# Kernel tuning notes

Measured on AMD Instinct MI355X. Metric: run time of the kernel, lower is better.

The kernel has to match this reference:

```python
import jax, jax.numpy as jnp
import numpy as np

N_NODES = 40000
N_EDGES = 480000
MULT = 64
NUM_SPECIES = 5
N_BASIS = 8
MLP_HIDDEN = 64
AVG_NEIGH = 12.0

INV8 = float(1.0 / np.sqrt(8.0))
INV64 = float(1.0 / np.sqrt(64.0))
INV128 = float(1.0 / np.sqrt(128.0))


def _poly_envelope(x):
    # e3nn.poly_envelope(5, 2) == DimeNet-style cutoff with p=6:
    # f(0)=1, first 5 derivatives zero at 0, f and 2 derivatives zero at 1.
    u = 1.0 - 28.0 * x**6 + 48.0 * x**7 - 21.0 * x**8
    return jnp.where(x < 1.0, u, 0.0)


def setup_inputs() -> dict:
    key = jax.random.key(0)
    ks = jax.random.split(key, 15)
    vectors = jax.random.uniform(ks[0], (N_EDGES, 3), jnp.float32, -0.5, 0.5)
    node_scalars = jax.random.normal(ks[1], (N_NODES, MULT), jnp.float32)
    node_vectors = jax.random.normal(ks[2], (N_NODES, MULT, 3), jnp.float32)
    node_specie = jax.random.randint(ks[3], (N_NODES,), 0, NUM_SPECIES)
    senders = jax.random.randint(ks[4], (N_EDGES,), 0, N_NODES)
    receivers = jax.random.randint(ks[5], (N_EDGES,), 0, N_NODES)
    # learned params (e3nn Linear weights ~ N(0,1), fwd divides by sqrt(fan_in))
    W_up_s = jax.random.normal(ks[6], (MULT, MULT), jnp.float32)
    W_up_v = jax.random.normal(ks[7], (MULT, MULT), jnp.float32)
    W_skip_s = jax.random.normal(ks[8], (NUM_SPECIES, MULT, 2 * MULT), jnp.float32)
    W_skip_v = jax.random.normal(ks[9], (NUM_SPECIES, MULT, MULT), jnp.float32)
    W_mlp1 = jax.random.normal(ks[10], (N_BASIS, MLP_HIDDEN), jnp.float32)
    W_mlp2 = jax.random.normal(ks[11], (MLP_HIDDEN, MLP_HIDDEN), jnp.float32)
    W_mlp3 = jax.random.normal(ks[12], (MLP_HIDDEN, 4 * MULT), jnp.float32)
    W_down_s = jax.random.normal(ks[13], (2 * MULT, 2 * MULT), jnp.float32)
    W_down_v = jax.random.normal(ks[14], (2 * MULT, MULT), jnp.float32)
    return dict(vectors=vectors, node_scalars=node_scalars, node_vectors=node_vectors,
                node_specie=node_specie, senders=senders, receivers=receivers,
                W_up_s=W_up_s, W_up_v=W_up_v, W_skip_s=W_skip_s, W_skip_v=W_skip_v,
                W_mlp1=W_mlp1, W_mlp2=W_mlp2, W_mlp3=W_mlp3,
                W_down_s=W_down_s, W_down_v=W_down_v)


def reference(vectors, node_scalars, node_vectors, node_specie, senders, receivers,
              W_up_s, W_up_v, W_skip_s, W_skip_v, W_mlp1, W_mlp2, W_mlp3,
              W_down_s, W_down_v):
    N = node_scalars.shape[0]
    # self-connection: species-indexed linear ('skip_tp'), output 128x0e + 64x1o
    sc_s = jnp.einsum('ni,nio->no', node_scalars, W_skip_s[node_specie]) * INV64
    sc_v = jnp.einsum('nic,nio->noc', node_vectors, W_skip_v[node_specie]) * INV64
    # linear_up (irreps-wise linear, 64x0e+64x1o -> same)
    h_s = (node_scalars @ W_up_s) * INV64
    h_v = jnp.einsum('nic,io->noc', node_vectors, W_up_v) * INV64
    # gather by sender
    m_s = h_s[senders]                       # [E,64]
    m_v = h_v[senders]                       # [E,64,3]
    # spherical harmonics l=1, normalize=True, component norm: sqrt(3)*r_hat
    lengths = jnp.linalg.norm(vectors, axis=1, keepdims=True)   # [E,1]
    safe_len = jnp.where(lengths == 0.0, 1.0, lengths)
    Y = jnp.sqrt(3.0) * vectors / safe_len                      # [E,3]
    # sparse CG tensor product (component norm): 0e x 1o -> 1o, 1o x 1o -> 0e
    tp_1o = m_s[:, :, None] * Y[:, None, :]                     # [E,64,3]
    tp_0e = jnp.einsum('eic,ec->ei', m_v, Y) / jnp.sqrt(3.0)    # [E,64]
    # concatenate + regroup -> 128x0e + 128x1o
    msg_s = jnp.concatenate([m_s, tp_0e], axis=1)               # [E,128]
    msg_v = jnp.concatenate([m_v, tp_1o], axis=1)               # [E,128,3]
    # radial basis (bessel, x_max=1) * smooth envelope
    k = jnp.arange(1, N_BASIS + 1, dtype=jnp.float32)
    bes = jnp.sqrt(2.0) * jnp.sin(k * jnp.pi * safe_len) / safe_len  # [E,8]
    rb = jnp.where(lengths == 0.0, 0.0, bes * _poly_envelope(lengths))
    h = jax.nn.swish((rb @ W_mlp1) * INV8)
    h = jax.nn.swish((h @ W_mlp2) * INV64)
    mix = (h @ W_mlp3) * INV64                                  # [E,256]
    msg_s = msg_s * mix[:, :128]
    msg_v = msg_v * mix[:, 128:, None]
    # scatter-add to receivers, normalize by sqrt(avg_num_neighbors)
    inv_sqrt_nn = 1.0 / np.sqrt(AVG_NEIGH)
    agg_s = jax.ops.segment_sum(msg_s, receivers, num_segments=N) * inv_sqrt_nn
    agg_v = jax.ops.segment_sum(msg_v, receivers, num_segments=N) * inv_sqrt_nn
    # linear_down to 128x0e + 64x1o, plus self-connection
    d_s = (agg_s @ W_down_s) * INV128 + sc_s                    # [N,128]
    d_v = jnp.einsum('nic,io->noc', agg_v, W_down_v) * INV128 + sc_v  # [N,64,3]
    # gate: first 64 scalars kept (swish), last 64 gate the vectors (swish)
    out_s = jax.nn.swish(d_s[:, :MULT])
    gates = jax.nn.swish(d_s[:, MULT:])
    out_v = d_v * gates[:, :, None]
    return jnp.concatenate([out_s, out_v.reshape(N, MULT * 3)], axis=1)  # [N,256]
```

## Files before the change

### kernel.cpp

```cpp
#include <hip/hip_runtime.h>
#include <hip/hip_bf16.h>

#define N_NODES 40000
#define N_EDGES 480000
#define SEG 2
#define SEG_E (N_EDGES / SEG)
#define SEG_TILES (SEG_E / 16)
#define SCAN_BLOCKS 157
#define TPW 4

typedef short bf16x8 __attribute__((ext_vector_type(8)));
typedef float f32x4 __attribute__((ext_vector_type(4)));

__device__ __forceinline__ float bf2f(__hip_bfloat16 x) { return __bfloat162float(x); }

__device__ __forceinline__ float swishf(float x) { return x / (1.0f + __expf(-x)); }

__device__ __forceinline__ float bflo(unsigned u) { union { unsigned u; float f; } w; w.u = u << 16; return w.f; }
__device__ __forceinline__ float bfhi(unsigned u) { union { unsigned u; float f; } w; w.u = u & 0xffff0000u; return w.f; }
__device__ __forceinline__ float bfu(unsigned short u) { union { unsigned u; float f; } w; w.u = ((unsigned)u) << 16; return w.f; }

__device__ __forceinline__ unsigned short f2bf_bits(float x) {
    union { __hip_bfloat16 h; unsigned short u; } c; c.h = __float2bfloat16(x); return c.u;
}

__constant__ const float INV8 = 0.35355339059327373f;
__constant__ const float INV64 = 0.125f;
__constant__ const float INV128 = 0.08838834764831845f;
__constant__ const float INV_NN = 0.2886751345948129f;
__constant__ const float SQRT2 = 1.4142135623730951f;
__constant__ const float SQRT3 = 1.7320508075688772f;
__constant__ const float INV_SQRT3 = 0.5773502691896258f;
__constant__ const float PI_F = 3.14159265358979323846f;

__device__ __forceinline__ float LDf(const void* p, size_t i, bool f32) {
    float v;
    if (f32) v = ((const float*)p)[i];
    else     v = bf2f(((const __hip_bfloat16*)p)[i]);
    return v;
}
__device__ __forceinline__ void load_f8r(const void* p, size_t i, bool f32, float* out) {
    if (f32) {
        const float4* q4 = (const float4*)((const float*)p + i);
        float4 a = q4[0], b = q4[1];
        out[0] = a.x; out[1] = a.y; out[2] = a.z; out[3] = a.w;
        out[4] = b.x; out[5] = b.y; out[6] = b.z; out[7] = b.w;
    } else {
        bf16x8 v = *(const bf16x8*)((const unsigned short*)p + i);
        #pragma unroll
        for (int j = 0; j < 8; j++) out[j] = bfu((unsigned short)v[j]);
    }
}

__global__ void detect_kernel(const unsigned short* __restrict__ w, int* __restrict__ flag) {
    int lane = threadIdx.x;
    int cnt = 0;
    for (int i = lane; i < 2048; i += 64) {
        unsigned e = (w[2 * i] >> 7) & 0xFF;
        if (e >= 110 && e <= 133) cnt++;
    }
    #pragma unroll
    for (int off = 32; off > 0; off >>= 1) cnt += __shfl_down(cnt, off, 64);
    if (lane == 0) *flag = (cnt > 1024) ? 1 : 0;
}

__global__ __launch_bounds__(256) void wprep_kernel(
    const void* __restrict__ W_up_s, const void* __restrict__ W_up_v,
    const void* __restrict__ W_skip_s, const void* __restrict__ W_skip_v,
    const void* __restrict__ W_down_s, const void* __restrict__ W_down_v,
    const void* __restrict__ W_mlp2, const void* __restrict__ W_mlp3,
    unsigned short* __restrict__ Wup_sq, unsigned short* __restrict__ Wup_vq,
    unsigned short* __restrict__ Wq_s, unsigned short* __restrict__ Wq_v,
    unsigned short* __restrict__ W2q, unsigned short* __restrict__ W3q,
    const int* __restrict__ flag)
{
    bool f32 = (*flag == 0);
    const float SC = INV128 * INV_NN;
    int gid = blockIdx.x * 256 + threadIdx.x;
    int gs = gridDim.x * 256;
    for (int i = gid; i < 4096; i += gs) {
        int o = i & 63, k = i >> 6;
        Wup_sq[o * 72 + k] = f2bf_bits(LDf(W_up_s, k * 64 + o, f32) * INV64);
        Wup_vq[o * 72 + k] = f2bf_bits(LDf(W_up_v, k * 64 + o, f32) * INV64);
    }
    for (int i = gid; i < 5 * 128 * 192; i += gs) {
        int sp = i / 24576, r = i - sp * 24576;
        int o = r / 192, k = r - o * 192;
        float w = (k < 128) ? LDf(W_down_s, k * 128 + o, f32) * SC
                            : LDf(W_skip_s, sp * 8192 + (k - 128) * 128 + o, f32) * INV64;
        Wq_s[sp * 25600 + o * 200 + k] = f2bf_bits(w);
    }
    for (int i = gid; i < 5 * 64 * 192; i += gs) {
        int sp = i / 12288, r = i - sp * 12288;
        int o = r / 192, k = r - o * 192;
        float w = (k < 128) ? LDf(W_down_v, k * 64 + o, f32) * SC
                            : LDf(W_skip_v, sp * 4096 + (k - 128) * 64 + o, f32) * INV64;
        Wq_v[sp * 12800 + o * 200 + k] = f2bf_bits(w);
    }
    for (int i = gid; i < 16384; i += gs) {
        int o = i & 255, k = i >> 8;
        W3q[o * 72 + k] = f2bf_bits(LDf(W_mlp3, k * 256 + o, f32));
    }
    for (int i = gid; i < 4096; i += gs) {
        int o = i & 63, k = i >> 6;
        W2q[o * 72 + k] = f2bf_bits(LDf(W_mlp2, k * 64 + o, f32));
    }
}

__global__ __launch_bounds__(256) void hist_kernel(const int* __restrict__ receivers,
                                                   int* __restrict__ cnt) {
    int e = blockIdx.x * 256 + threadIdx.x;
    if (e < N_EDGES) atomicAdd(&cnt[receivers[e]], 1);
}

__global__ __launch_bounds__(256) void partial_kernel(const int* __restrict__ cnt,
                                                      int* __restrict__ partials) {
    __shared__ int red[4];
    int idx = blockIdx.x * 256 + threadIdx.x;
    int v = (idx < N_NODES) ? cnt[idx] : 0;
    #pragma unroll
    for (int off = 32; off > 0; off >>= 1) v += __shfl_down(v, off, 64);
    int wave = threadIdx.x >> 6, lane = threadIdx.x & 63;
    if (lane == 0) red[wave] = v;
    __syncthreads();
    if (threadIdx.x == 0) partials[blockIdx.x] = red[0] + red[1] + red[2] + red[3];
}

__global__ __launch_bounds__(256) void scanp_kernel(const int* __restrict__ partials,
                                                    int* __restrict__ pscan) {
    __shared__ int buf[256];
    int t = threadIdx.x;
    int v = (t < SCAN_BLOCKS) ? partials[t] : 0;
    buf[t] = v;
    __syncthreads();
    for (int off = 1; off < 256; off <<= 1) {
        int tmp = (t >= off) ? buf[t - off] : 0;
        __syncthreads();
        buf[t] += tmp;
        __syncthreads();
    }
    if (t < SCAN_BLOCKS) pscan[t] = buf[t] - v;
}

__global__ __launch_bounds__(256) void offs_kernel(const int* __restrict__ cnt,
                                                   const int* __restrict__ pscan,
                                                   int* __restrict__ offs,
                                                   int* __restrict__ cursor) {
    __shared__ int buf[256];
    int b = blockIdx.x, t = threadIdx.x;
    int idx = b * 256 + t;
    int v = (idx < N_NODES) ? cnt[idx] : 0;
    buf[t] = v;
    __syncthreads();
    for (int off = 1; off < 256; off <<= 1) {
        int tmp = (t >= off) ? buf[t - off] : 0;
        __syncthreads();
        buf[t] += tmp;
        __syncthreads();
    }
    int exc = buf[t] - v + pscan[b];
    if (idx < N_NODES) { offs[idx] = exc; cursor[idx] = exc; }
    if (idx == N_NODES - 1) offs[N_NODES] = exc + v;
}

__global__ __launch_bounds__(256) void scatter_kernel(const int* __restrict__ receivers,
                                                      const int* __restrict__ senders,
                                                      const void* __restrict__ vectors,
                                                      int* __restrict__ cursor,
                                                      int* __restrict__ sorted_snd,
                                                      unsigned short* __restrict__ yq,
                                                      unsigned short* __restrict__ rbq,
                                                      const int* __restrict__ flag) {
    bool f32 = (*flag == 0);
    int e = blockIdx.x * 256 + threadIdx.x;
    if (e < N_EDGES) {
        float vx = LDf(vectors, (size_t)e * 3 + 0, f32);
        float vy = LDf(vectors, (size_t)e * 3 + 1, f32);
        float vz = LDf(vectors, (size_t)e * 3 + 2, f32);
        float len2 = vx * vx + vy * vy + vz * vz;
        float len = sqrtf(len2);
        float Yx = 0.f, Yy = 0.f, Yz = 0.f;
        float rb[8];
        if (len > 0.f) {
            float inv = 1.f / len;
            Yx = SQRT3 * vx * inv; Yy = SQRT3 * vy * inv; Yz = SQRT3 * vz * inv;
            float x6 = len2 * len2 * len2;
            float env = (len < 1.f) ? fmaf(x6, fmaf(len, fmaf(len, -21.f, 48.f), -28.f), 1.f) : 0.f;
            float c = SQRT2 * inv * env;
            #pragma unroll
            for (int k = 0; k < 8; k++) rb[k] = c * __sinf((float)(k + 1) * PI_F * len);
        } else {
            #pragma unroll
            for (int k = 0; k < 8; k++) rb[k] = 0.f;
        }
        int p = atomicAdd(&cursor[receivers[e]], 1);
        sorted_snd[p] = senders[e];
        uint2 yw;
        yw.x = f2bf_bits(Yx) | ((unsigned)f2bf_bits(Yy) << 16);
        yw.y = f2bf_bits(Yz);
        *(uint2*)(yq + (size_t)p * 4) = yw;
        bf16x8 r8;
        #pragma unroll
        for (int k = 0; k < 8; k++) r8[k] = (short)f2bf_bits(rb[k]);
        *(bf16x8*)(rbq + (size_t)p * 8) = r8;
    }
}

__global__ __launch_bounds__(256) void hist5_kernel(const int* __restrict__ specie,
                                                    int* __restrict__ cnt5) {
    int n = blockIdx.x * 256 + threadIdx.x;
    int lane = threadIdx.x & 63;
    int sp = (n < N_NODES) ? specie[n] : -1;
    #pragma unroll
    for (int s = 0; s < 5; s++) {
        unsigned long long mask = __ballot(sp == s);
        if (mask != 0ull) {
            int leader = __builtin_ctzll(mask);
            if (lane == leader) atomicAdd(&cnt5[s], __popcll(mask));
        }
    }
}

__global__ void scan5_kernel(const int* __restrict__ cnt5, int* __restrict__ sp_offs,
                             int* __restrict__ cursor5, int* __restrict__ tile_info) {
    if (threadIdx.x != 0 || blockIdx.x != 0) return;
    int run = 0, tb = 0;
    for (int s = 0; s < 5; s++) {
        sp_offs[s] = run; cursor5[s] = run;
        tile_info[s] = tb;
        int c = cnt5[s];
        int T = (c + 15) >> 4;
        tile_info[8 + s] = T;
        tb += (T + 3) >> 2;
        run += c;
    }
    sp_offs[5] = run;
    tile_info[5] = tb;
}

__global__ __launch_bounds__(256) void scatter5_kernel(const int* __restrict__ specie,
                                                       int* __restrict__ cursor5,
                                                       int* __restrict__ sorted_node) {
    int n = blockIdx.x * 256 + threadIdx.x;
    int lane = threadIdx.x & 63;
    int sp = (n < N_NODES) ? specie[n] : -1;
    #pragma unroll
    for (int s = 0; s < 5; s++) {
        unsigned long long mask = __ballot(sp == s);
        if (mask != 0ull) {
            int leader = __builtin_ctzll(mask);
            int base = 0;
            if (lane == leader) base = atomicAdd(&cursor5[s], __popcll(mask));
            base = __shfl(base, leader);
            if (sp == s) {
                int prefix = __popcll(mask & ((1ull << lane) - 1ull));
                sorted_node[base + prefix] = n;
            }
        }
    }
}

__global__ __launch_bounds__(256) void node_up_kernel(
    const void* __restrict__ node_scalars,
    const void* __restrict__ node_vectors,
    const unsigned short* __restrict__ Wup_sq,
    const unsigned short* __restrict__ Wup_vq,
    unsigned short* __restrict__ hbuf,
    unsigned short* __restrict__ ns_b,
    unsigned short* __restrict__ nv_t,
    const int* __restrict__ flag)
{
    bool f32 = (*flag == 0);
    __shared__ __align__(16) unsigned short WsT[64 * 72];
    __shared__ __align__(16) unsigned short WvT[64 * 72];
    int tid = threadIdx.x;
    for (int i = tid; i < 576; i += 256) {
        ((uint4*)WsT)[i] = ((const uint4*)Wup_sq)[i];
        ((uint4*)WvT)[i] = ((const uint4*)Wup_vq)[i];
    }
    __syncthreads();
    int wave = tid >> 6, lane = tid & 63;
    int m = lane & 15, q = lane >> 4;
    int base = (blockIdx.x * 4 + wave) * 16;

    f32x4 accS[4];
    f32x4 accV[3][4];
    #pragma unroll
    for (int t = 0; t < 4; t++) {
        accS[t] = f32x4{0.f, 0.f, 0.f, 0.f};
        #pragma unroll
        for (int c = 0; c < 3; c++) accV[c][t] = f32x4{0.f, 0.f, 0.f, 0.f};
    }

    #pragma unroll
    for (int kk = 0; kk < 2; kk++) {
        int i0 = kk * 32 + 8 * q;
        float fs[8];
        load_f8r(node_scalars, (size_t)(base + m) * 64 + i0, f32, fs);
        bf16x8 aS;
        #pragma unroll
        for (int j = 0; j < 8; j++) aS[j] = (short)f2bf_bits(fs[j]);
        *(bf16x8*)(ns_b + (size_t)(base + m) * 64 + i0) = aS;
        float fv[24];
        size_t vbase = (size_t)(base + m) * 192 + (size_t)i0 * 3;
        load_f8r(node_vectors, vbase,      f32, fv);
        load_f8r(node_vectors, vbase + 8,  f32, fv + 8);
        load_f8r(node_vectors, vbase + 16, f32, fv + 16);
        bf16x8 aV[3];
        #pragma unroll
        for (int c = 0; c < 3; c++) {
            #pragma unroll
            for (int j = 0; j < 8; j++) aV[c][j] = (short)f2bf_bits(fv[3 * j + c]);
            *(bf16x8*)(nv_t + (size_t)c * N_NODES * 64 + (size_t)(base + m) * 64 + i0) = aV[c];
        }
        #pragma unroll
        for (int t = 0; t < 4; t++) {
            bf16x8 bS = *(const bf16x8*)(WsT + (16 * t + m) * 72 + kk * 32 + 8 * q);
            bf16x8 bV = *(const bf16x8*)(WvT + (16 * t + m) * 72 + kk * 32 + 8 * q);
            accS[t]    = __builtin_amdgcn_mfma_f32_16x16x32_bf16(aS,    bS, accS[t],    0, 0, 0);
            accV[0][t] = __builtin_amdgcn_mfma_f32_16x16x32_bf16(aV[0], bV, accV[0][t], 0, 0, 0);
            accV[1][t] = __builtin_amdgcn_mfma_f32_16x16x32_bf16(aV[1], bV, accV[1][t], 0, 0, 0);
            accV[2][t] = __builtin_amdgcn_mfma_f32_16x16x32_bf16(aV[2], bV, accV[2][t], 0, 0, 0);
        }
    }
    #pragma unroll
    for (int t = 0; t < 4; t++) {
        #pragma unroll
        for (int r = 0; r < 4; r++) {
            uint2 pk;
            pk.x = (unsigned)f2bf_bits(accS[t][r])    | ((unsigned)f2bf_bits(accV[0][t][r]) << 16);
            pk.y = (unsigned)f2bf_bits(accV[1][t][r]) | ((unsigned)f2bf_bits(accV[2][t][r]) << 16);
            *(uint2*)(hbuf + (size_t)(base + 4 * q + r) * 256 + (16 * t + m) * 4) = pk;
        }
    }
}

__global__ __launch_bounds__(512) void mlp_kernel(
    const unsigned short* __restrict__ rbq,
    const void* __restrict__ W1,
    const unsigned short* __restrict__ W2q,
    const unsigned short* __restrict__ W3q,
    unsigned short* __restrict__ mixp,
    int p_lo,
    const int* __restrict__ flag)
{
    bool f32 = (*flag == 0);
    __shared__ __align__(16) unsigned short W3T[256 * 72];
    __shared__ __align__(16) unsigned short W2T[64 * 72];
    __shared__ unsigned short hbl[8 * 64 * 18];
    int tid = threadIdx.x;
    for (int i = tid; i < 2304; i += 512) ((uint4*)W3T)[i] = ((const uint4*)W3q)[i];
    for (int i = tid; i < 576; i += 512)  ((uint4*)W2T)[i] = ((const uint4*)W2q)[i];
    __syncthreads();
    int wave = tid >> 6, lane = tid & 63;
    int m = lane & 15, q = lane >> 4;
    unsigned short* hb = hbl + wave * (64 * 18);
    f32x4 zero4 = {0.f, 0.f, 0.f, 0.f};

    bf16x8 a1f[4];
    #pragma unroll
    for (int t = 0; t < 4; t++) {
        #pragma unroll
        for (int j = 0; j < 8; j++) a1f[t][j] = 0;
        if (q == 0) {
            #pragma unroll
            for (int j = 0; j < 8; j++)
                a1f[t][j] = (short)f2bf_bits(LDf(W1, j * 64 + 16 * t + m, f32));
        }
    }

    int tile0 = (blockIdx.x * 8 + wave) * TPW;
    #pragma unroll 1
    for (int tt = 0; tt < TPW; tt++) {
        int tile = tile0 + tt;
        if (tile >= SEG_TILES) break;
        int p = p_lo + tile * 16 + m;

        bf16x8 b_rb;
        #pragma unroll
        for (int j = 0; j < 8; j++) b_rb[j] = 0;
        if (q == 0) b_rb = *(const bf16x8*)(rbq + (size_t)p * 8);

        #pragma unroll
        for (int t = 0; t < 4; t++) {
            f32x4 c = __builtin_amdgcn_mfma_f32_16x16x32_bf16(a1f[t], b_rb, zero4, 0, 0, 0);
            #pragma unroll
            for (int r = 0; r < 4; r++)
                hb[(16 * t + 4 * q + r) * 18 + m] = f2bf_bits(swishf(c[r] * INV8));
        }
        bf16x8 b2[2];
        #pragma unroll
        for (int h = 0; h < 2; h++)
            #pragma unroll
            for (int j = 0; j < 8; j++)
                b2[h][j] = (short)hb[(32 * h + 8 * q + j) * 18 + m];
        #pragma unroll
        for (int t = 0; t < 4; t++) {
            bf16x8 a0 = *(const bf16x8*)(W2T + (16 * t + m) * 72 + 8 * q);
            bf16x8 a1 = *(const bf16x8*)(W2T + (16 * t + m) * 72 + 32 + 8 * q);
            f32x4 c = __builtin_amdgcn_mfma_f32_16x16x32_bf16(a0, b2[0], zero4, 0, 0, 0);
            c = __builtin_amdgcn_mfma_f32_16x16x32_bf16(a1, b2[1], c, 0, 0, 0);
            #pragma unroll
            for (int r = 0; r < 4; r++)
                hb[(16 * t + 4 * q + r) * 18 + m] = f2bf_bits(swishf(c[r] * INV64));
        }
        bf16x8 b3[2];
        #pragma unroll
        for (int h = 0; h < 2; h++)
            #pragma unroll
            for (int j = 0; j < 8; j++)
                b3[h][j] = (short)hb[(32 * h + 8 * q + j) * 18 + m];
        size_t ebase = ((size_t)(tile * 16 + m)) * 256;
        #pragma unroll
        for (int t3p = 0; t3p < 4; t3p++) {
            f32x4 cg[4];
            #pragma unroll
            for (int g = 0; g < 4; g++) {
                int t3 = t3p + 4 * g;
                bf16x8 a0 = *(const bf16x8*)(W3T + (16 * t3 + m) * 72 + 8 * q);
                bf16x8 a1 = *(const bf16x8*)(W3T + (16 * t3 + m) * 72 + 32 + 8 * q);
                f32x4 c = __builtin_amdgcn_mfma_f32_16x16x32_bf16(a0, b3[0], zero4, 0, 0, 0);
                cg[g] = __builtin_amdgcn_mfma_f32_16x16x32_bf16(a1, b3[1], c, 0, 0, 0);
            }
            #pragma unroll
            for (int r = 0; r < 4; r += 2) {
                uint4 w;
                w.x = f2bf_bits(cg[0][r] * INV64)     | ((unsigned)f2bf_bits(cg[1][r] * INV64) << 16);
                w.y = f2bf_bits(cg[2][r] * INV64)     | ((unsigned)f2bf_bits(cg[3][r] * INV64) << 16);
                w.z = f2bf_bits(cg[0][r + 1] * INV64) | ((unsigned)f2bf_bits(cg[1][r + 1] * INV64) << 16);
                w.w = f2bf_bits(cg[2][r + 1] * INV64) | ((unsigned)f2bf_bits(cg[3][r + 1] * INV64) << 16);
                *(uint4*)(mixp + ebase + (size_t)(16 * t3p + 4 * q + r) * 4) = w;
            }
        }
    }
}

__global__ __launch_bounds__(256) void agg_kernel(
    const unsigned short* __restrict__ hbuf,
    const int* __restrict__ sorted_snd,
    const unsigned short* __restrict__ mixp,
    const unsigned short* __restrict__ yq,
    const int* __restrict__ offs,
    unsigned short* __restrict__ agg_s_b,
    unsigned short* __restrict__ agg_v_b,
    int slo, int shi)
{
    int tid = threadIdx.x, wave = tid >> 6, lane = tid & 63;
    int n = blockIdx.x * 4 + wave;
    if (n >= N_NODES) return;
    int beg = __builtin_amdgcn_readfirstlane(offs[n]);
    int end = __builtin_amdgcn_readfirstlane(offs[n + 1]);
    int lo = beg > slo ? beg : slo;
    int hi = end < shi ? end : shi;
    bool owner = (beg >= slo && beg < shi) || (beg >= shi && shi == N_EDGES);
    if (!owner && hi <= lo) return;
    unsigned short* aS = agg_s_b + (size_t)n * 128;
    unsigned short* aV = agg_v_b + (size_t)n * 384;
    float s0, s1, v0, v1, v2, v3, v4, v5;
    if (owner) {
        s0 = s1 = v0 = v1 = v2 = v3 = v4 = v5 = 0.f;
    } else {
        s0 = bfu(aS[lane]); s1 = bfu(aS[64 + lane]);
        v0 = bfu(aV[lane]); v1 = bfu(aV[64 + lane]); v2 = bfu(aV[128 + lane]);
        v3 = bfu(aV[192 + lane]); v4 = bfu(aV[256 + lane]); v5 = bfu(aV[320 + lane]);
    }
    for (int chunk = lo; chunk < hi; chunk += 64) {
        int cc = hi - chunk; if (cc > 64) cc = 64;
        int sv = (lane < cc) ? sorted_snd[chunk + lane] : 0;
        int i = 0;
        for (; i + 3 < cc; i += 4) {
            uint2 h[4], mxw[4], yw[4];
            #pragma unroll
            for (int u = 0; u < 4; u++) {
                int snd = __builtin_amdgcn_readlane(sv, i + u);
                int p = chunk + i + u;
                h[u]   = *(const uint2*)(hbuf + (size_t)snd * 256 + lane * 4);
                mxw[u] = *(const uint2*)(mixp + (size_t)(p - slo) * 256 + lane * 4);
                yw[u]  = *(const uint2*)(yq + (size_t)p * 4);
            }
            #pragma unroll
            for (int u = 0; u < 4; u++) {
                float m_s = bflo(h[u].x), mv0 = bfhi(h[u].x), mv1 = bflo(h[u].y), mv2 = bfhi(h[u].y);
                float mix0 = bflo(mxw[u].x), mix1 = bfhi(mxw[u].x);
                float mix2 = bflo(mxw[u].y), mix3 = bfhi(mxw[u].y);
                float Yx = bflo(yw[u].x), Yy = bfhi(yw[u].x), Yz = bflo(yw[u].y);
                float tp0 = (mv0 * Yx + mv1 * Yy + mv2 * Yz) * INV_SQRT3;
                s0 = fmaf(m_s, mix0, s0);
                s1 = fmaf(tp0, mix1, s1);
                float t1 = m_s * mix3;
                v0 = fmaf(mv0, mix2, v0); v1 = fmaf(t1, Yx, v1);
                v2 = fmaf(mv1, mix2, v2); v3 = fmaf(t1, Yy, v3);
                v4 = fmaf(mv2, mix2, v4); v5 = fmaf(t1, Yz, v5);
            }
        }
        for (; i < cc; i++) {
            int snd = __builtin_amdgcn_readlane(sv, i);
            int p = chunk + i;
            uint2 hbv = *(const uint2*)(hbuf + (size_t)snd * 256 + lane * 4);
            uint2 mxw = *(const uint2*)(mixp + (size_t)(p - slo) * 256 + lane * 4);
            uint2 yw  = *(const uint2*)(yq + (size_t)p * 4);
            float m_s = bflo(hbv.x), mv0 = bfhi(hbv.x), mv1 = bflo(hbv.y), mv2 = bfhi(hbv.y);
            float mix0 = bflo(mxw.x), mix1 = bfhi(mxw.x);
            float mix2 = bflo(mxw.y), mix3 = bfhi(mxw.y);
            float Yx = bflo(yw.x), Yy = bfhi(yw.x), Yz = bflo(yw.y);
            float tp0 = (mv0 * Yx + mv1 * Yy + mv2 * Yz) * INV_SQRT3;
            s0 = fmaf(m_s, mix0, s0);
            s1 = fmaf(tp0, mix1, s1);
            float t1 = m_s * mix3;
            v0 = fmaf(mv0, mix2, v0); v1 = fmaf(t1, Yx, v1);
            v2 = fmaf(mv1, mix2, v2); v3 = fmaf(t1, Yy, v3);
            v4 = fmaf(mv2, mix2, v4); v5 = fmaf(t1, Yz, v5);
        }
    }
    aS[lane] = f2bf_bits(s0); aS[64 + lane] = f2bf_bits(s1);
    aV[lane] = f2bf_bits(v0); aV[64 + lane] = f2bf_bits(v1); aV[128 + lane] = f2bf_bits(v2);
    aV[192 + lane] = f2bf_bits(v3); aV[256 + lane] = f2bf_bits(v4); aV[320 + lane] = f2bf_bits(v5);
}

__global__ __launch_bounds__(256) void node_final_kernel(
    const unsigned short* __restrict__ Wq_s,
    const unsigned short* __restrict__ Wq_v,
    const unsigned short* __restrict__ ns_b,
    const unsigned short* __restrict__ nv_t,
    const unsigned short* __restrict__ agg_s_b,
    const unsigned short* __restrict__ agg_v_b,
    const int* __restrict__ sorted_node,
    const int* __restrict__ sp_offs,
    const int* __restrict__ tile_info,
    void* __restrict__ out,
    const int* __restrict__ flag)
{
    bool f32 = (*flag == 0);
    int b = blockIdx.x;
    if (b >= tile_info[5]) return;
    __shared__ __align__(16) unsigned short As[128 * 200];
    __shared__ __align__(16) unsigned short Av[64 * 200];
    int sp = 0;
    #pragma unroll
    for (int s = 1; s < 5; s++) if (b >= tile_info[s]) sp = s;
    int tid = threadIdx.x;
    const uint4* ps = (const uint4*)(Wq_s + (size_t)sp * 25600);
    for (int i = tid; i < 3200; i += 256) ((uint4*)As)[i] = ps[i];
    const uint4* pv = (const uint4*)(Wq_v + (size_t)sp * 12800);
    for (int i = tid; i < 1600; i += 256) ((uint4*)Av)[i] = pv[i];
    __syncthreads();
    int wave = tid >> 6, lane = tid & 63;
    int m = lane & 15, q = lane >> 4;
    int T = tile_info[8 + sp];
    int tl = (b - tile_info[sp]) * 4 + wave;
    if (tl >= T) return;
    int row = sp_offs[sp] + tl * 16;
    int cnt = sp_offs[sp + 1] - row; if (cnt > 16) cnt = 16;
    int mm = (m < cnt) ? m : 0;
    int node = sorted_node[row + mm];

    bf16x8 bs[6];
    {
        const unsigned short* a = agg_s_b + (size_t)node * 128;
        #pragma unroll
        for (int f = 0; f < 4; f++) bs[f] = *(const bf16x8*)(a + f * 32 + q * 8);
        const unsigned short* s = ns_b + (size_t)node * 64;
        #pragma unroll
        for (int f = 0; f < 2; f++) bs[4 + f] = *(const bf16x8*)(s + f * 32 + q * 8);
    }
    bf16x8 bv[3][6];
    #pragma unroll
    for (int c = 0; c < 3; c++) {
        const unsigned short* a = agg_v_b + (size_t)node * 384 + c * 128;
        #pragma unroll
        for (int f = 0; f < 4; f++) bv[c][f] = *(const bf16x8*)(a + f * 32 + q * 8);
        const unsigned short* s = nv_t + (size_t)c * N_NODES * 64 + (size_t)node * 64;
        #pragma unroll
        for (int f = 0; f < 2; f++) bv[c][4 + f] = *(const bf16x8*)(s + f * 32 + q * 8);
    }
    f32x4 z4 = {0.f, 0.f, 0.f, 0.f};
    float gate[4][4];
    #pragma unroll
    for (int t = 0; t < 4; t++) {
        f32x4 c = z4;
        #pragma unroll
        for (int f = 0; f < 6; f++) {
            bf16x8 a = *(const bf16x8*)(As + (16 * (4 + t) + m) * 200 + f * 32 + q * 8);
            c = __builtin_amdgcn_mfma_f32_16x16x32_bf16(a, bs[f], c, 0, 0, 0);
        }
        #pragma unroll
        for (int r = 0; r < 4; r++) gate[t][r] = swishf(c[r]);
    }
    #pragma unroll
    for (int t = 0; t < 4; t++) {
        f32x4 c = z4;
        #pragma unroll
        for (int f = 0; f < 6; f++) {
            bf16x8 a = *(const bf16x8*)(As + (16 * t + m) * 200 + f * 32 + q * 8);
            c = __builtin_amdgcn_mfma_f32_16x16x32_bf16(a, bs[f], c, 0, 0, 0);
        }
        if (m < cnt) {
            size_t base = (size_t)node * 256 + 16 * t + 4 * q;
            if (f32) {
                float4 o4 = { swishf(c[0]), swishf(c[1]), swishf(c[2]), swishf(c[3]) };
                *(float4*)((float*)out + base) = o4;
            } else {
                uint2 o2;
                o2.x = f2bf_bits(swishf(c[0])) | ((unsigned)f2bf_bits(swishf(c[1])) << 16);
                o2.y = f2bf_bits(swishf(c[2])) | ((unsigned)f2bf_bits(swishf(c[3])) << 16);
                *(uint2*)((unsigned short*)out + base) = o2;
            }
        }
    }
    #pragma unroll
    for (int t = 0; t < 4; t++) {
        f32x4 c0 = z4, c1 = z4, c2 = z4;
        #pragma unroll
        for (int f = 0; f < 6; f++) {
            bf16x8 a = *(const bf16x8*)(Av + (16 * t + m) * 200 + f * 32 + q * 8);
            c0 = __builtin_amdgcn_mfma_f32_16x16x32_bf16(a, bv[0][f], c0, 0, 0, 0);
            c1 = __builtin_amdgcn_mfma_f32_16x16x32_bf16(a, bv[1][f], c1, 0, 0, 0);
            c2 = __builtin_amdgcn_mfma_f32_16x16x32_bf16(a, bv[2][f], c2, 0, 0, 0);
        }
        if (m < cnt) {
            #pragma unroll
            for (int r = 0; r < 4; r++) {
                float g = gate[t][r];
                int o = 16 * t + 4 * q + r;
                size_t base = (size_t)node * 256 + 64 + (size_t)o * 3;
                if (f32) {
                    ((float*)out)[base + 0] = c0[r] * g;
                    ((float*)out)[base + 1] = c1[r] * g;
                    ((float*)out)[base + 2] = c2[r] * g;
                } else {
                    ((__hip_bfloat16*)out)[base + 0] = __float2bfloat16(c0[r] * g);
                    ((__hip_bfloat16*)out)[base + 1] = __float2bfloat16(c1[r] * g);
                    ((__hip_bfloat16*)out)[base + 2] = __float2bfloat16(c2[r] * g);
                }
            }
        }
    }
}

extern "C" void kernel_launch(void* const* d_in, const int* in_sizes, int n_in,
                              void* d_out, int out_size, void* d_ws, size_t ws_size,
                              hipStream_t stream) {
    const void* vectors      = d_in[0];
    const void* node_scalars = d_in[1];
    const void* node_vectors = d_in[2];
    const int* node_specie   = (const int*)d_in[3];
    const int* senders       = (const int*)d_in[4];
    const int* receivers     = (const int*)d_in[5];
    const void* W_up_s       = d_in[6];
    const void* W_up_v       = d_in[7];
    const void* W_skip_s     = d_in[8];
    const void* W_skip_v     = d_in[9];
    const void* W_mlp1       = d_in[10];
    const void* W_mlp2       = d_in[11];
    const void* W_mlp3       = d_in[12];
    const void* W_down_s     = d_in[13];
    const void* W_down_v     = d_in[14];

    char* ws = (char*)d_ws;
    size_t off = 0;
    auto alloc = [&](size_t bytes) { void* p = ws + off; off += (bytes + 255) & ~(size_t)255; return p; };
    unsigned short* hbuf     = (unsigned short*)alloc((size_t)N_NODES * 256 * 2);
    unsigned short* ns_b     = (unsigned short*)alloc((size_t)N_NODES * 64 * 2);
    unsigned short* nv_t     = (unsigned short*)alloc((size_t)N_NODES * 192 * 2);
    unsigned short* agg_s_b  = (unsigned short*)alloc((size_t)N_NODES * 128 * 2);
    unsigned short* agg_v_b  = (unsigned short*)alloc((size_t)N_NODES * 384 * 2);
    unsigned short* mixp     = (unsigned short*)alloc((size_t)SEG_E * 256 * 2);
    unsigned short* yq       = (unsigned short*)alloc((size_t)N_EDGES * 4 * 2);
    unsigned short* rbq      = (unsigned short*)alloc((size_t)N_EDGES * 8 * 2);
    unsigned short* Wup_sq   = (unsigned short*)alloc((size_t)64 * 72 * 2);
    unsigned short* Wup_vq   = (unsigned short*)alloc((size_t)64 * 72 * 2);
    unsigned short* Wq_s     = (unsigned short*)alloc((size_t)5 * 128 * 200 * 2);
    unsigned short* Wq_v     = (unsigned short*)alloc((size_t)5 * 64 * 200 * 2);
    unsigned short* W2q      = (unsigned short*)alloc((size_t)64 * 72 * 2);
    unsigned short* W3q      = (unsigned short*)alloc((size_t)256 * 72 * 2);
    int* cnt        = (int*)alloc((size_t)(N_NODES + 8) * 4);
    int* cnt5       = cnt + N_NODES;
    int* offs       = (int*)alloc((size_t)(N_NODES + 1) * 4);
    int* cursor     = (int*)alloc((size_t)N_NODES * 4);
    int* sorted_snd = (int*)alloc((size_t)N_EDGES * 4);
    int* sorted_node= (int*)alloc((size_t)N_NODES * 4);
    int* sp_offs    = (int*)alloc(16 * 4);
    int* cursor5    = (int*)alloc(16 * 4);
    int* tile_info  = (int*)alloc(16 * 4);
    int* partials   = (int*)alloc((size_t)(SCAN_BLOCKS + 1) * 4);
    int* pscan      = (int*)alloc((size_t)(SCAN_BLOCKS + 1) * 4);
    int* flag       = (int*)alloc(4);

    detect_kernel<<<dim3(1), dim3(64), 0, stream>>>((const unsigned short*)W_up_s, flag);
    (void)hipMemsetAsync(cnt, 0, (size_t)(N_NODES + 8) * 4, stream);

    wprep_kernel<<<dim3(64), dim3(256), 0, stream>>>(
        W_up_s, W_up_v, W_skip_s, W_skip_v, W_down_s, W_down_v, W_mlp2, W_mlp3,
        Wup_sq, Wup_vq, Wq_s, Wq_v, W2q, W3q, flag);

    hist_kernel<<<dim3(1875), dim3(256), 0, stream>>>(receivers, cnt);
    partial_kernel<<<dim3(SCAN_BLOCKS), dim3(256), 0, stream>>>(cnt, partials);
    scanp_kernel<<<dim3(1), dim3(256), 0, stream>>>(partials, pscan);
    offs_kernel<<<dim3(SCAN_BLOCKS), dim3(256), 0, stream>>>(cnt, pscan, offs, cursor);
    scatter_kernel<<<dim3(1875), dim3(256), 0, stream>>>(receivers, senders, vectors,
                                                         cursor, sorted_snd, yq, rbq, flag);

    hist5_kernel<<<dim3(157), dim3(256), 0, stream>>>(node_specie, cnt5);
    scan5_kernel<<<dim3(1), dim3(64), 0, stream>>>(cnt5, sp_offs, cursor5, tile_info);
    scatter5_kernel<<<dim3(157), dim3(256), 0, stream>>>(node_specie, cursor5, sorted_node);

    node_up_kernel<<<dim3(625), dim3(256), 0, stream>>>(
        node_scalars, node_vectors, Wup_sq, Wup_vq, hbuf, ns_b, nv_t, flag);

    const int MLP_BLOCKS = (SEG_TILES + 8 * TPW - 1) / (8 * TPW);
    for (int s = 0; s < SEG; s++) {
        int p_lo = s * SEG_E;
        mlp_kernel<<<dim3(MLP_BLOCKS), dim3(512), 0, stream>>>(
            rbq, W_mlp1, W2q, W3q, mixp, p_lo, flag);
        agg_kernel<<<dim3(10000), dim3(256), 0, stream>>>(
            hbuf, sorted_snd, mixp, yq, offs, agg_s_b, agg_v_b, p_lo, p_lo + SEG_E);
    }

    node_final_kernel<<<dim3(640), dim3(256), 0, stream>>>(
        Wq_s, Wq_v, ns_b, nv_t, agg_s_b, agg_v_b,
        sorted_node, sp_offs, tile_info, d_out, flag);
}
```

Before: 489.3 us.

## Fuse radial MLP with edge aggregation using per-receiver run atomics

Merges the edge MLP kernel and the per-node aggregation kernel into one pass over receiver-sorted edge tiles. The mix coefficients stay in LDS instead of going through a global mixp buffer, and each wave accumulates runs of equal receivers and flushes them to fp32 global accumulators with atomicAdd. This removes the mixp write/read round trip and the two-segment launch loop. In exchange it adds a 80MB fp32 memset, a sorted_rcv array and atomics at tile boundaries, and the final kernel now reads fp32 aggregates.

After: 529.5 us. +8.2%, slower.

```diff
diff --git a/kernel.cpp b/kernel.cpp
--- a/kernel.cpp
+++ b/kernel.cpp
@@ -3,9 +3,7 @@
 
 #define N_NODES 40000
 #define N_EDGES 480000
-#define SEG 2
-#define SEG_E (N_EDGES / SEG)
-#define SEG_TILES (SEG_E / 16)
+#define N_TILES (N_EDGES / 16)
 #define SCAN_BLOCKS 157
 #define TPW 4
 
@@ -50,6 +48,15 @@
         #pragma unroll
         for (int j = 0; j < 8; j++) out[j] = bfu((unsigned short)v[j]);
     }
+}
+__device__ __forceinline__ bf16x8 packf8(const float* p) {
+    float4 x = ((const float4*)p)[0], y = ((const float4*)p)[1];
+    bf16x8 r;
+    r[0] = (short)f2bf_bits(x.x); r[1] = (short)f2bf_bits(x.y);
+    r[2] = (short)f2bf_bits(x.z); r[3] = (short)f2bf_bits(x.w);
+    r[4] = (short)f2bf_bits(y.x); r[5] = (short)f2bf_bits(y.y);
+    r[6] = (short)f2bf_bits(y.z); r[7] = (short)f2bf_bits(y.w);
+    return r;
 }
 
 __global__ void detect_kernel(const unsigned short* __restrict__ w, int* __restrict__ flag) {
@@ -168,6 +175,7 @@
                                                       const void* __restrict__ vectors,
                                                       int* __restrict__ cursor,
                                                       int* __restrict__ sorted_snd,
+                                                      int* __restrict__ sorted_rcv,
                                                       unsigned short* __restrict__ yq,
                                                       unsigned short* __restrict__ rbq,
                                                       const int* __restrict__ flag) {
@@ -193,8 +201,10 @@
             #pragma unroll
             for (int k = 0; k < 8; k++) rb[k] = 0.f;
         }
-        int p = atomicAdd(&cursor[receivers[e]], 1);
+        int rcv = receivers[e];
+        int p = atomicAdd(&cursor[rcv], 1);
         sorted_snd[p] = senders[e];
+        sorted_rcv[p] = rcv;
         uint2 yw;
         yw.x = f2bf_bits(Yx) | ((unsigned)f2bf_bits(Yy) << 16);
         yw.y = f2bf_bits(Yz);
@@ -335,26 +345,30 @@
     }
 }
 
-__global__ __launch_bounds__(512) void mlp_kernel(
+__global__ __launch_bounds__(256) void fused_kernel(
     const unsigned short* __restrict__ rbq,
     const void* __restrict__ W1,
     const unsigned short* __restrict__ W2q,
     const unsigned short* __restrict__ W3q,
-    unsigned short* __restrict__ mixp,
-    int p_lo,
+    const unsigned short* __restrict__ hbuf,
+    const int* __restrict__ sorted_snd,
+    const int* __restrict__ sorted_rcv,
+    const unsigned short* __restrict__ yq,
+    float* __restrict__ agg_s_f,
+    float* __restrict__ agg_v_f,
     const int* __restrict__ flag)
 {
     bool f32 = (*flag == 0);
     __shared__ __align__(16) unsigned short W3T[256 * 72];
-    __shared__ __align__(16) unsigned short W2T[64 * 72];
-    __shared__ unsigned short hbl[8 * 64 * 18];
+    __shared__ unsigned short hbl[4 * 64 * 17];
+    __shared__ unsigned short mixt[4 * 256 * 17];
     int tid = threadIdx.x;
-    for (int i = tid; i < 2304; i += 512) ((uint4*)W3T)[i] = ((const uint4*)W3q)[i];
-    for (int i = tid; i < 576; i += 512)  ((uint4*)W2T)[i] = ((const uint4*)W2q)[i];
+    for (int i = tid; i < 2304; i += 256) ((uint4*)W3T)[i] = ((const uint4*)W3q)[i];
     __syncthreads();
     int wave = tid >> 6, lane = tid & 63;
     int m = lane & 15, q = lane >> 4;
-    unsigned short* hb = hbl + wave * (64 * 18);
+    unsigned short* hb = hbl + wave * (64 * 17);
+    unsigned short* mt = mixt + wave * (256 * 17);
     f32x4 zero4 = {0.f, 0.f, 0.f, 0.f};
 
     bf16x8 a1f[4];
@@ -368,13 +382,21 @@
                 a1f[t][j] = (short)f2bf_bits(LDf(W1, j * 64 + 16 * t + m, f32));
         }
     }
-
-    int tile0 = (blockIdx.x * 8 + wave) * TPW;
+    bf16x8 w2f[4][2];
+    #pragma unroll
+    for (int t = 0; t < 4; t++) {
+        w2f[t][0] = *(const bf16x8*)(W2q + (16 * t + m) * 72 + 8 * q);
+        w2f[t][1] = *(const bf16x8*)(W2q + (16 * t + m) * 72 + 32 + 8 * q);
+    }
+
+    float s0 = 0.f, s1 = 0.f, v0 = 0.f, v1 = 0.f, v2 = 0.f, v3 = 0.f, v4 = 0.f, v5 = 0.f;
+    int cur = -1;
+
     #pragma unroll 1
     for (int tt = 0; tt < TPW; tt++) {
-        int tile = tile0 + tt;
-        if (tile >= SEG_TILES) break;
-        int p = p_lo + tile * 16 + m;
+        int tile = (blockIdx.x * 4 + wave) * TPW + tt;
+        int p0 = tile * 16;
+        int p = p0 + m;
 
         bf16x8 b_rb;
         #pragma unroll
@@ -386,31 +408,28 @@
             f32x4 c = __builtin_amdgcn_mfma_f32_16x16x32_bf16(a1f[t], b_rb, zero4, 0, 0, 0);
             #pragma unroll
             for (int r = 0; r < 4; r++)
-                hb[(16 * t + 4 * q + r) * 18 + m] = f2bf_bits(swishf(c[r] * INV8));
+                hb[(16 * t + 4 * q + r) * 17 + m] = f2bf_bits(swishf(c[r] * INV8));
         }
         bf16x8 b2[2];
         #pragma unroll
         for (int h = 0; h < 2; h++)
             #pragma unroll
             for (int j = 0; j < 8; j++)
-                b2[h][j] = (short)hb[(32 * h + 8 * q + j) * 18 + m];
+                b2[h][j] = (short)hb[(32 * h + 8 * q + j) * 17 + m];
         #pragma unroll
         for (int t = 0; t < 4; t++) {
-            bf16x8 a0 = *(const bf16x8*)(W2T + (16 * t + m) * 72 + 8 * q);
-            bf16x8 a1 = *(const bf16x8*)(W2T + (16 * t + m) * 72 + 32 + 8 * q);
-            f32x4 c = __builtin_amdgcn_mfma_f32_16x16x32_bf16(a0, b2[0], zero4, 0, 0, 0);
-            c = __builtin_amdgcn_mfma_f32_16x16x32_bf16(a1, b2[1], c, 0, 0, 0);
+            f32x4 c = __builtin_amdgcn_mfma_f32_16x16x32_bf16(w2f[t][0], b2[0], zero4, 0, 0, 0);
+            c = __builtin_amdgcn_mfma_f32_16x16x32_bf16(w2f[t][1], b2[1], c, 0, 0, 0);
             #pragma unroll
             for (int r = 0; r < 4; r++)
-                hb[(16 * t + 4 * q + r) * 18 + m] = f2bf_bits(swishf(c[r] * INV64));
+                hb[(16 * t + 4 * q + r) * 17 + m] = f2bf_bits(swishf(c[r] * INV64));
         }
         bf16x8 b3[2];
         #pragma unroll
         for (int h = 0; h < 2; h++)
             #pragma unroll
             for (int j = 0; j < 8; j++)
-                b3[h][j] = (short)hb[(32 * h + 8 * q + j) * 18 + m];
-        size_t ebase = ((size_t)(tile * 16 + m)) * 256;
+                b3[h][j] = (short)hb[(32 * h + 8 * q + j) * 17 + m];
         #pragma unroll
         for (int t3p = 0; t3p < 4; t3p++) {
             f32x4 cg[4];
@@ -423,85 +442,40 @@
                 cg[g] = __builtin_amdgcn_mfma_f32_16x16x32_bf16(a1, b3[1], c, 0, 0, 0);
             }
             #pragma unroll
-            for (int r = 0; r < 4; r += 2) {
-                uint4 w;
-                w.x = f2bf_bits(cg[0][r] * INV64)     | ((unsigned)f2bf_bits(cg[1][r] * INV64) << 16);
-                w.y = f2bf_bits(cg[2][r] * INV64)     | ((unsigned)f2bf_bits(cg[3][r] * INV64) << 16);
-                w.z = f2bf_bits(cg[0][r + 1] * INV64) | ((unsigned)f2bf_bits(cg[1][r + 1] * INV64) << 16);
-                w.w = f2bf_bits(cg[2][r + 1] * INV64) | ((unsigned)f2bf_bits(cg[3][r + 1] * INV64) << 16);
-                *(uint4*)(mixp + ebase + (size_t)(16 * t3p + 4 * q + r) * 4) = w;
+            for (int g = 0; g < 4; g++)
+                #pragma unroll
+                for (int r = 0; r < 4; r++)
+                    mt[((16 * t3p + 4 * q + r) * 4 + g) * 17 + m] = f2bf_bits(cg[g][r] * INV64);
+        }
+
+        int sv = sorted_snd[p];
+        int rv = sorted_rcv[p];
+        #pragma unroll 4
+        for (int i = 0; i < 16; i++) {
+            int rcv = __builtin_amdgcn_readlane(rv, i);
+            int snd = __builtin_amdgcn_readlane(sv, i);
+            if (rcv != cur) {
+                if (cur >= 0) {
+                    atomicAdd(&agg_s_f[(size_t)cur * 128 + lane], s0);
+                    atomicAdd(&agg_s_f[(size_t)cur * 128 + 64 + lane], s1);
+                    float* av = agg_v_f + (size_t)cur * 384;
+                    atomicAdd(&av[lane], v0);
+                    atomicAdd(&av[64 + lane], v1);
+                    atomicAdd(&av[128 + lane], v2);
+                    atomicAdd(&av[192 + lane], v3);
+                    atomicAdd(&av[256 + lane], v4);
+                    atomicAdd(&av[320 + lane], v5);
+                }
+                s0 = s1 = v0 = v1 = v2 = v3 = v4 = v5 = 0.f;
+                cur = rcv;
             }
-        }
-    }
-}
-
-__global__ __launch_bounds__(256) void agg_kernel(
-    const unsigned short* __restrict__ hbuf,
-    const int* __restrict__ sorted_snd,
-    const unsigned short* __restrict__ mixp,
-    const unsigned short* __restrict__ yq,
-    const int* __restrict__ offs,
-    unsigned short* __restrict__ agg_s_b,
-    unsigned short* __restrict__ agg_v_b,
-    int slo, int shi)
-{
-    int tid = threadIdx.x, wave = tid >> 6, lane = tid & 63;
-    int n = blockIdx.x * 4 + wave;
-    if (n >= N_NODES) return;
-    int beg = __builtin_amdgcn_readfirstlane(offs[n]);
-    int end = __builtin_amdgcn_readfirstlane(offs[n + 1]);
-    int lo = beg > slo ? beg : slo;
-    int hi = end < shi ? end : shi;
-    bool owner = (beg >= slo && beg < shi) || (beg >= shi && shi == N_EDGES);
-    if (!owner && hi <= lo) return;
-    unsigned short* aS = agg_s_b + (size_t)n * 128;
-    unsigned short* aV = agg_v_b + (size_t)n * 384;
-    float s0, s1, v0, v1, v2, v3, v4, v5;
-    if (owner) {
-        s0 = s1 = v0 = v1 = v2 = v3 = v4 = v5 = 0.f;
-    } else {
-        s0 = bfu(aS[lane]); s1 = bfu(aS[64 + lane]);
-        v0 = bfu(aV[lane]); v1 = bfu(aV[64 + lane]); v2 = bfu(aV[128 + lane]);
-        v3 = bfu(aV[192 + lane]); v4 = bfu(aV[256 + lane]); v5 = bfu(aV[320 + lane]);
-    }
-    for (int chunk = lo; chunk < hi; chunk += 64) {
-        int cc = hi - chunk; if (cc > 64) cc = 64;
-        int sv = (lane < cc) ? sorted_snd[chunk + lane] : 0;
-        int i = 0;
-        for (; i + 3 < cc; i += 4) {
-            uint2 h[4], mxw[4], yw[4];
-            #pragma unroll
-            for (int u = 0; u < 4; u++) {
-                int snd = __builtin_amdgcn_readlane(sv, i + u);
-                int p = chunk + i + u;
-                h[u]   = *(const uint2*)(hbuf + (size_t)snd * 256 + lane * 4);
-                mxw[u] = *(const uint2*)(mixp + (size_t)(p - slo) * 256 + lane * 4);
-                yw[u]  = *(const uint2*)(yq + (size_t)p * 4);
-            }
-            #pragma unroll
-            for (int u = 0; u < 4; u++) {
-                float m_s = bflo(h[u].x), mv0 = bfhi(h[u].x), mv1 = bflo(h[u].y), mv2 = bfhi(h[u].y);
-                float mix0 = bflo(mxw[u].x), mix1 = bfhi(mxw[u].x);
-                float mix2 = bflo(mxw[u].y), mix3 = bfhi(mxw[u].y);
-                float Yx = bflo(yw[u].x), Yy = bfhi(yw[u].x), Yz = bflo(yw[u].y);
-                float tp0 = (mv0 * Yx + mv1 * Yy + mv2 * Yz) * INV_SQRT3;
-                s0 = fmaf(m_s, mix0, s0);
-                s1 = fmaf(tp0, mix1, s1);
-                float t1 = m_s * mix3;
-                v0 = fmaf(mv0, mix2, v0); v1 = fmaf(t1, Yx, v1);
-                v2 = fmaf(mv1, mix2, v2); v3 = fmaf(t1, Yy, v3);
-                v4 = fmaf(mv2, mix2, v4); v5 = fmaf(t1, Yz, v5);
-            }
-        }
-        for (; i < cc; i++) {
-            int snd = __builtin_amdgcn_readlane(sv, i);
-            int p = chunk + i;
             uint2 hbv = *(const uint2*)(hbuf + (size_t)snd * 256 + lane * 4);
-            uint2 mxw = *(const uint2*)(mixp + (size_t)(p - slo) * 256 + lane * 4);
-            uint2 yw  = *(const uint2*)(yq + (size_t)p * 4);
+            uint2 yw  = *(const uint2*)(yq + (size_t)(p0 + i) * 4);
+            float mix0 = bfu(mt[(lane * 4 + 0) * 17 + i]);
+            float mix1 = bfu(mt[(lane * 4 + 1) * 17 + i]);
+            float mix2 = bfu(mt[(lane * 4 + 2) * 17 + i]);
+            float mix3 = bfu(mt[(lane * 4 + 3) * 17 + i]);
             float m_s = bflo(hbv.x), mv0 = bfhi(hbv.x), mv1 = bflo(hbv.y), mv2 = bfhi(hbv.y);
-            float mix0 = bflo(mxw.x), mix1 = bfhi(mxw.x);
-            float mix2 = bflo(mxw.y), mix3 = bfhi(mxw.y);
             float Yx = bflo(yw.x), Yy = bfhi(yw.x), Yz = bflo(yw.y);
             float tp0 = (mv0 * Yx + mv1 * Yy + mv2 * Yz) * INV_SQRT3;
             s0 = fmaf(m_s, mix0, s0);
@@ -512,9 +486,17 @@
             v4 = fmaf(mv2, mix2, v4); v5 = fmaf(t1, Yz, v5);
         }
     }
-    aS[lane] = f2bf_bits(s0); aS[64 + lane] = f2bf_bits(s1);
-    aV[lane] = f2bf_bits(v0); aV[64 + lane] = f2bf_bits(v1); aV[128 + lane] = f2bf_bits(v2);
-    aV[192 + lane] = f2bf_bits(v3); aV[256 + lane] = f2bf_bits(v4); aV[320 + lane] = f2bf_bits(v5);
+    if (cur >= 0) {
+        atomicAdd(&agg_s_f[(size_t)cur * 128 + lane], s0);
+        atomicAdd(&agg_s_f[(size_t)cur * 128 + 64 + lane], s1);
+        float* av = agg_v_f + (size_t)cur * 384;
+        atomicAdd(&av[lane], v0);
+        atomicAdd(&av[64 + lane], v1);
+        atomicAdd(&av[128 + lane], v2);
+        atomicAdd(&av[192 + lane], v3);
+        atomicAdd(&av[256 + lane], v4);
+        atomicAdd(&av[320 + lane], v5);
+    }
 }
 
 __global__ __launch_bounds__(256) void node_final_kernel(
@@ -522,8 +504,8 @@
     const unsigned short* __restrict__ Wq_v,
     const unsigned short* __restrict__ ns_b,
     const unsigned short* __restrict__ nv_t,
-    const unsigned short* __restrict__ agg_s_b,
-    const unsigned short* __restrict__ agg_v_b,
+    const float* __restrict__ agg_s_f,
+    const float* __restrict__ agg_v_f,
     const int* __restrict__ sorted_node,
     const int* __restrict__ sp_offs,
     const int* __restrict__ tile_info,
@@ -556,9 +538,9 @@
 
     bf16x8 bs[6];
     {
-        const unsigned short* a = agg_s_b + (size_t)node * 128;
-        #pragma unroll
-        for (int f = 0; f < 4; f++) bs[f] = *(const bf16x8*)(a + f * 32 + q * 8);
+        const float* a = agg_s_f + (size_t)node * 128;
+        #pragma unroll
+        for (int f = 0; f < 4; f++) bs[f] = packf8(a + f * 32 + q * 8);
         const unsigned short* s = ns_b + (size_t)node * 64;
         #pragma unroll
         for (int f = 0; f < 2; f++) bs[4 + f] = *(const bf16x8*)(s + f * 32 + q * 8);
@@ -566,9 +548,9 @@
     bf16x8 bv[3][6];
     #pragma unroll
     for (int c = 0; c < 3; c++) {
-        const unsigned short* a = agg_v_b + (size_t)node * 384 + c * 128;
-        #pragma unroll
-        for (int f = 0; f < 4; f++) bv[c][f] = *(const bf16x8*)(a + f * 32 + q * 8);
+        const float* a = agg_v_f + (size_t)node * 384 + c * 128;
+        #pragma unroll
+        for (int f = 0; f < 4; f++) bv[c][f] = packf8(a + f * 32 + q * 8);
         const unsigned short* s = nv_t + (size_t)c * N_NODES * 64 + (size_t)node * 64;
         #pragma unroll
         for (int f = 0; f < 2; f++) bv[c][4 + f] = *(const bf16x8*)(s + f * 32 + q * 8);
@@ -662,9 +644,9 @@
     unsigned short* hbuf     = (unsigned short*)alloc((size_t)N_NODES * 256 * 2);
     unsigned short* ns_b     = (unsigned short*)alloc((size_t)N_NODES * 64 * 2);
     unsigned short* nv_t     = (unsigned short*)alloc((size_t)N_NODES * 192 * 2);
-    unsigned short* agg_s_b  = (unsigned short*)alloc((size_t)N_NODES * 128 * 2);
-    unsigned short* agg_v_b  = (unsigned short*)alloc((size_t)N_NODES * 384 * 2);
-    unsigned short* mixp     = (unsigned short*)alloc((size_t)SEG_E * 256 * 2);
+    float* agg_f             = (float*)alloc((size_t)N_NODES * 512 * 4);
+    float* agg_s_f           = agg_f;
+    float* agg_v_f           = agg_f + (size_t)N_NODES * 128;
     unsigned short* yq       = (unsigned short*)alloc((size_t)N_EDGES * 4 * 2);
     unsigned short* rbq      = (unsigned short*)alloc((size_t)N_EDGES * 8 * 2);
     unsigned short* Wup_sq   = (unsigned short*)alloc((size_t)64 * 72 * 2);
@@ -678,6 +660,7 @@
     int* offs       = (int*)alloc((size_t)(N_NODES + 1) * 4);
     int* cursor     = (int*)alloc((size_t)N_NODES * 4);
     int* sorted_snd = (int*)alloc((size_t)N_EDGES * 4);
+    int* sorted_rcv = (int*)alloc((size_t)N_EDGES * 4);
     int* sorted_node= (int*)alloc((size_t)N_NODES * 4);
     int* sp_offs    = (int*)alloc(16 * 4);
     int* cursor5    = (int*)alloc(16 * 4);
@@ -688,6 +671,7 @@
 
     detect_kernel<<<dim3(1), dim3(64), 0, stream>>>((const unsigned short*)W_up_s, flag);
     (void)hipMemsetAsync(cnt, 0, (size_t)(N_NODES + 8) * 4, stream);
+    (void)hipMemsetAsync(agg_f, 0, (size_t)N_NODES * 512 * 4, stream);
 
     wprep_kernel<<<dim3(64), dim3(256), 0, stream>>>(
         W_up_s, W_up_v, W_skip_s, W_skip_v, W_down_s, W_down_v, W_mlp2, W_mlp3,
@@ -698,7 +682,7 @@
     scanp_kernel<<<dim3(1), dim3(256), 0, stream>>>(partials, pscan);
     offs_kernel<<<dim3(SCAN_BLOCKS), dim3(256), 0, stream>>>(cnt, pscan, offs, cursor);
     scatter_kernel<<<dim3(1875), dim3(256), 0, stream>>>(receivers, senders, vectors,
-                                                         cursor, sorted_snd, yq, rbq, flag);
+                                                         cursor, sorted_snd, sorted_rcv, yq, rbq, flag);
 
     hist5_kernel<<<dim3(157), dim3(256), 0, stream>>>(node_specie, cnt5);
     scan5_kernel<<<dim3(1), dim3(64), 0, stream>>>(cnt5, sp_offs, cursor5, tile_info);
@@ -707,16 +691,11 @@
     node_up_kernel<<<dim3(625), dim3(256), 0, stream>>>(
         node_scalars, node_vectors, Wup_sq, Wup_vq, hbuf, ns_b, nv_t, flag);
 
-    const int MLP_BLOCKS = (SEG_TILES + 8 * TPW - 1) / (8 * TPW);
-    for (int s = 0; s < SEG; s++) {
-        int p_lo = s * SEG_E;
-        mlp_kernel<<<dim3(MLP_BLOCKS), dim3(512), 0, stream>>>(
-            rbq, W_mlp1, W2q, W3q, mixp, p_lo, flag);
-        agg_kernel<<<dim3(10000), dim3(256), 0, stream>>>(
-            hbuf, sorted_snd, mixp, yq, offs, agg_s_b, agg_v_b, p_lo, p_lo + SEG_E);
-    }
+    const int FUSED_BLOCKS = N_TILES / (4 * TPW);
+    fused_kernel<<<dim3(FUSED_BLOCKS), dim3(256), 0, stream>>>(
+        rbq, W_mlp1, W2q, W3q, hbuf, sorted_snd, sorted_rcv, yq, agg_s_f, agg_v_f, flag);
 
     node_final_kernel<<<dim3(640), dim3(256), 0, stream>>>(
-        Wq_s, Wq_v, ns_b, nv_t, agg_s_b, agg_v_b,
+        Wq_s, Wq_v, ns_b, nv_t, agg_s_f, agg_v_f,
         sorted_node, sp_offs, tile_info, d_out, flag);
 }
```
